# Kernel optimization log

Measured on AMD Instinct MI355X. Metric: run time of the kernel, lower is better.

The kernel has to match this reference:

```python
import jax, jax.numpy as jnp
import numpy as np

B, T, U = 4, 256, 64
D_ENC = D_PRED = 512
JOINT = 1024
VOCAB = 1024


def setup_inputs() -> dict:
    key = jax.random.key(0)
    ks = jax.random.split(key, 8)
    s = lambda d: 1.0 / np.sqrt(d)
    return {
        "enc": jax.random.normal(ks[0], (B, T, D_ENC), jnp.float32),
        "pred": jax.random.normal(ks[1], (B, U, D_PRED), jnp.float32),
        "W_enc": jax.random.normal(ks[2], (D_ENC, JOINT), jnp.float32) * s(D_ENC),
        "b_enc": jnp.zeros((JOINT,), jnp.float32),
        "W_pred": jax.random.normal(ks[3], (D_PRED, JOINT), jnp.float32) * s(D_PRED),
        "b_pred": jnp.zeros((JOINT,), jnp.float32),
        "W_out": jax.random.normal(ks[4], (JOINT, VOCAB), jnp.float32) * s(JOINT),
        "b_out": jnp.zeros((VOCAB,), jnp.float32),
    }


def reference(enc, pred, W_enc, b_enc, W_pred, b_pred, W_out, b_out):
    # Dense projections to joint_dim
    enc_out = jnp.einsum("btd,dj->btj", enc, W_enc) + b_enc      # [B,T,J]
    pred_out = jnp.einsum("bud,dj->buj", pred, W_pred) + b_pred  # [B,U,J]
    # Broadcast add over (T,U), tanh, then vocab projection
    joint = jnp.tanh(enc_out[:, :, None, :] + pred_out[:, None, :, :])  # [B,T,U,J]
    logits = jnp.einsum("btuj,jv->btuv", joint, W_out) + b_out           # [B,T,U,V]
    return logits
```

## Files before the change

kernel.cpp:

```cpp
#include <hip/hip_runtime.h>
#include <hip/hip_bf16.h>


typedef __bf16 bf16x8 __attribute__((ext_vector_type(8)));
typedef float f32x4 __attribute__((ext_vector_type(4)));
typedef unsigned int u32x4 __attribute__((ext_vector_type(4)));
using bf16_t = __hip_bfloat16;

#define B_ 4
#define T_ 256
#define U_ 64
#define DE 512
#define JD 1024
#define VV 1024

__device__ __forceinline__ void gl2lds16(const void* g, void* l) {
  __builtin_amdgcn_global_load_lds(
      (__attribute__((address_space(1))) void*)(g),
      (__attribute__((address_space(3))) void*)(l), 16, 0, 0);
}

__device__ __forceinline__ float fast_tanh(float x) {
  float xx = fminf(fmaxf(x, -30.f), 30.f);
  float e = __expf(2.f * xx);
  return 1.f - 2.f * __builtin_amdgcn_rcpf(e + 1.f);
}

__global__ void cvt_bf16_k(const float* __restrict__ src, bf16_t* __restrict__ dst, int n) {
  int i = (blockIdx.x * blockDim.x + threadIdx.x) * 4;
  if (i >= n) return;
  f32x4 v = *(const f32x4*)(src + i);
  bf16_t o[4];
#pragma unroll
  for (int z = 0; z < 4; ++z) o[z] = __float2bfloat16(v[z]);
  *(unsigned long long*)(dst + i) = *(unsigned long long*)o;
}

__global__ void transpose_cvt_k(const float* __restrict__ src, bf16_t* __restrict__ dst,
                                int K, int N) {
  __shared__ float tile[32][33];
  int nt = blockIdx.x * 32, kt = blockIdx.y * 32;
  int tx = threadIdx.x, ty = threadIdx.y;
#pragma unroll
  for (int i = 0; i < 4; ++i)
    tile[ty + i * 8][tx] = src[(size_t)(kt + ty + i * 8) * N + nt + tx];
  __syncthreads();
#pragma unroll
  for (int i = 0; i < 4; ++i)
    dst[(size_t)(nt + ty + i * 8) * K + kt + tx] = __float2bfloat16(tile[tx][ty + i * 8]);
}

__global__ __launch_bounds__(256) void tanh_mat_k(
    const float* __restrict__ enc_o,
    const float* __restrict__ pred_o,
    bf16_t* __restrict__ joint) {
  size_t i = ((size_t)blockIdx.x * 256 + threadIdx.x) * 8;
  const int m = (int)(i >> 10);
  const int j = (int)(i & 1023);
  const int enc_row  = m >> 6;
  const int pred_row = ((m >> 14) << 6) | (m & 63);
  const f32x4* pe = (const f32x4*)(enc_o  + (size_t)enc_row  * JD + j);
  const f32x4* pp = (const f32x4*)(pred_o + (size_t)pred_row * JD + j);
  bf16_t vals[8];
#pragma unroll
  for (int q = 0; q < 2; ++q) {
    f32x4 e = pe[q], p = pp[q];
#pragma unroll
    for (int z = 0; z < 4; ++z)
      vals[q * 4 + z] = __float2bfloat16(fast_tanh(e[z] + p[z]));
  }
  *(u32x4*)(void*)(joint + i) = *(const u32x4*)(const void*)vals;
}

__global__ __launch_bounds__(256) void proj_gemm_k(
    const bf16_t* __restrict__ A, const bf16_t* __restrict__ Bt,
    const float* __restrict__ bias, float* __restrict__ C, int M, int N, int K) {
  __shared__ bf16_t sA[128 * 32];
  __shared__ bf16_t sB[128 * 32];
  const int tid = threadIdx.x;
  const int wave = tid >> 6, lane = tid & 63;
  const int wm = wave >> 1, wn = wave & 1;
  const int m0 = blockIdx.y * 128, n0 = blockIdx.x * 128;

  f32x4 acc[4][4] = {};

  for (int k0 = 0; k0 < K; k0 += 32) {
    __syncthreads();
#pragma unroll
    for (int r = 0; r < 2; ++r) {
      const int base = (wave + 4 * r) * 1024;
      const int row  = (base >> 6) + (lane >> 2);
      const int kel  = (lane & 3) * 8;
      gl2lds16(A  + (size_t)(m0 + row) * K + k0 + kel, (char*)sA + base);
      gl2lds16(Bt + (size_t)(n0 + row) * K + k0 + kel, (char*)sB + base);
    }
    __syncthreads();
    bf16x8 af[4], bfr[4];
    const int kq = (lane >> 4) * 8;
#pragma unroll
    for (int i = 0; i < 4; ++i) {
      af[i]  = *(const bf16x8*)(const void*)(sA + (wm * 64 + i * 16 + (lane & 15)) * 32 + kq);
      bfr[i] = *(const bf16x8*)(const void*)(sB + (wn * 64 + i * 16 + (lane & 15)) * 32 + kq);
    }
#pragma unroll
    for (int i = 0; i < 4; ++i)
#pragma unroll
      for (int j = 0; j < 4; ++j)
        acc[i][j] = __builtin_amdgcn_mfma_f32_16x16x32_bf16(af[i], bfr[j], acc[i][j], 0, 0, 0);
  }

  float bv[4];
#pragma unroll
  for (int j = 0; j < 4; ++j) bv[j] = bias[n0 + wn * 64 + j * 16 + (lane & 15)];
#pragma unroll
  for (int i = 0; i < 4; ++i) {
    const int row = m0 + wm * 64 + i * 16 + ((lane >> 4) << 2);
#pragma unroll
    for (int j = 0; j < 4; ++j) {
      const int col = n0 + wn * 64 + j * 16 + (lane & 15);
#pragma unroll
      for (int rr = 0; rr < 4; ++rr)
        C[(size_t)(row + rr) * N + col] = acc[i][j][rr] + bv[j];
    }
  }
}


__device__ __forceinline__ void stage_vtile(const bf16_t* __restrict__ A,
                                            const bf16_t* __restrict__ Bt,
                                            int m0, int n0, int k0,
                                            char* buf, int wave, int lane) {
  char* ab = buf;
  char* bb = buf + 16384;
  const int rw = lane >> 2;
  const int cl = lane & 3;
#pragma unroll
  for (int g = 0; g < 2; ++g) {
    const int r  = g * 128 + wave * 16 + rw;
    const int cg = cl ^ ((r >> 1) & 3);
    gl2lds16(A  + (size_t)(m0 + r) * JD + k0 + cg * 8, ab + (g * 128 + wave * 16) * 64);
    gl2lds16(Bt + (size_t)(n0 + r) * JD + k0 + cg * 8, bb + (g * 128 + wave * 16) * 64);
  }
}

__global__ __launch_bounds__(512, 2) void vocab_gemm8_k(
    const bf16_t* __restrict__ A,
    const bf16_t* __restrict__ Bt,
    const float* __restrict__ bias,
    float* __restrict__ C) {
  __shared__ char smem[65536];
  const int tid  = threadIdx.x;
  const int wave = tid >> 6, lane = tid & 63;
  const int wm = wave >> 2, wn = wave & 3;

  const int nwg = gridDim.x;
  const int cpx = nwg >> 3;
  const int b   = blockIdx.x;
  const int lb  = (b & 7) * cpx + (b >> 3);
  const int n0  = (lb & 3) * 256;
  const int m0  = (lb >> 2) * 256;

  f32x4 acc[8][4] = {};

  const int NT = JD / 32;
  stage_vtile(A, Bt, m0, n0, 0,  smem,         wave, lane);
  stage_vtile(A, Bt, m0, n0, 32, smem + 32768, wave, lane);
  asm volatile("s_waitcnt vmcnt(4)" ::: "memory");
  __builtin_amdgcn_s_barrier();
  __builtin_amdgcn_sched_barrier(0);

  for (int t = 0; t < NT; ++t) {
    const char* ab = smem + (t & 1) * 32768;
    const char* bb = ab + 16384;
    const int kq = lane >> 4;

    bf16x8 bfr[4];
#pragma unroll
    for (int j = 0; j < 4; ++j) {
      const int rb = wn * 64 + j * 16 + (lane & 15);
      const int cb = kq ^ ((rb >> 1) & 3);
      bfr[j] = *(const bf16x8*)(const void*)(bb + rb * 64 + cb * 16);
    }
#pragma unroll
    for (int mh = 0; mh < 2; ++mh) {
      bf16x8 af[4];
#pragma unroll
      for (int i = 0; i < 4; ++i) {
        const int ra = wm * 128 + mh * 64 + i * 16 + (lane & 15);
        const int ca = kq ^ ((ra >> 1) & 3);
        af[i] = *(const bf16x8*)(const void*)(ab + ra * 64 + ca * 16);
      }
      __builtin_amdgcn_s_setprio(1);
#pragma unroll
      for (int i = 0; i < 4; ++i)
#pragma unroll
        for (int j = 0; j < 4; ++j)
          acc[mh * 4 + i][j] =
              __builtin_amdgcn_mfma_f32_16x16x32_bf16(af[i], bfr[j], acc[mh * 4 + i][j], 0, 0, 0);
      __builtin_amdgcn_s_setprio(0);
    }

    if (t + 1 < NT) {
      __builtin_amdgcn_sched_barrier(0);
      __builtin_amdgcn_s_barrier();
      if (t + 2 < NT) {
        stage_vtile(A, Bt, m0, n0, (t + 2) * 32, smem + (t & 1) * 32768, wave, lane);
        asm volatile("s_waitcnt vmcnt(4)" ::: "memory");
      } else {
        asm volatile("s_waitcnt vmcnt(0)" ::: "memory");
      }
      __builtin_amdgcn_s_barrier();
      __builtin_amdgcn_sched_barrier(0);
    }
  }

  float bv[4];
#pragma unroll
  for (int j = 0; j < 4; ++j) bv[j] = bias[n0 + wn * 64 + j * 16 + (lane & 15)];
#pragma unroll
  for (int i = 0; i < 8; ++i) {
    const int row = m0 + wm * 128 + i * 16 + ((lane >> 4) << 2);
#pragma unroll
    for (int j = 0; j < 4; ++j) {
      const int col = n0 + wn * 64 + j * 16 + (lane & 15);
#pragma unroll
      for (int rr = 0; rr < 4; ++rr)
        C[(size_t)(row + rr) * VV + col] = acc[i][j][rr] + bv[j];
    }
  }
}

__global__ __launch_bounds__(256) void joint_gemm_k(
    const float* __restrict__ enc_out,
    const float* __restrict__ pred_out,
    const bf16_t* __restrict__ Wt,
    const float* __restrict__ b_out,
    float* __restrict__ out) {
  __shared__ bf16_t sA[128 * 32];
  __shared__ bf16_t sB[128 * 32];
  const int tid = threadIdx.x;
  const int wave = tid >> 6, lane = tid & 63;
  const int wm = wave >> 1, wn = wave & 1;
  const int m0 = blockIdx.y * 128, n0 = blockIdx.x * 128;

  const int ar  = tid >> 1;
  const int ac0 = (tid & 1) * 16;
  const int m = m0 + ar;
  const int enc_row  = m >> 6;
  const int pred_row = ((m >> 14) << 6) | (m & 63);
  const float* pe_base = enc_out  + (size_t)enc_row  * JD + ac0;
  const float* pp_base = pred_out + (size_t)pred_row * JD + ac0;

  f32x4 acc[4][4] = {};

  for (int k0 = 0; k0 < JD; k0 += 32) {
    __syncthreads();
#pragma unroll
    for (int r = 0; r < 2; ++r) {
      const int base = (wave + 4 * r) * 1024;
      const int row  = (base >> 6) + (lane >> 2);
      const int kel  = (lane & 3) * 8;
      gl2lds16(Wt + (size_t)(n0 + row) * JD + k0 + kel, (char*)sB + base);
    }
    bf16_t vals[16];
    const f32x4* pe = (const f32x4*)(pe_base + k0);
    const f32x4* pp = (const f32x4*)(pp_base + k0);
#pragma unroll
    for (int q = 0; q < 4; ++q) {
      f32x4 e = pe[q], p = pp[q];
#pragma unroll
      for (int z = 0; z < 4; ++z)
        vals[q * 4 + z] = __float2bfloat16(fast_tanh(e[z] + p[z]));
    }
    u32x4* dstp = (u32x4*)(void*)((char*)sA + ar * 64 + ac0 * 2);
    dstp[0] = ((const u32x4*)(const void*)vals)[0];
    dstp[1] = ((const u32x4*)(const void*)vals)[1];
    __syncthreads();

    bf16x8 af[4], bfr[4];
    const int kq = (lane >> 4) * 8;
#pragma unroll
    for (int i = 0; i < 4; ++i) {
      af[i]  = *(const bf16x8*)(const void*)(sA + (wm * 64 + i * 16 + (lane & 15)) * 32 + kq);
      bfr[i] = *(const bf16x8*)(const void*)(sB + (wn * 64 + i * 16 + (lane & 15)) * 32 + kq);
    }
#pragma unroll
    for (int i = 0; i < 4; ++i)
#pragma unroll
      for (int j = 0; j < 4; ++j)
        acc[i][j] = __builtin_amdgcn_mfma_f32_16x16x32_bf16(af[i], bfr[j], acc[i][j], 0, 0, 0);
  }

  float bv[4];
#pragma unroll
  for (int j = 0; j < 4; ++j) bv[j] = b_out[n0 + wn * 64 + j * 16 + (lane & 15)];
#pragma unroll
  for (int i = 0; i < 4; ++i) {
    const int row = m0 + wm * 64 + i * 16 + ((lane >> 4) << 2);
#pragma unroll
    for (int j = 0; j < 4; ++j) {
      const int col = n0 + wn * 64 + j * 16 + (lane & 15);
#pragma unroll
      for (int rr = 0; rr < 4; ++rr)
        out[(size_t)(row + rr) * VV + col] = acc[i][j][rr] + bv[j];
    }
  }
}

extern "C" void kernel_launch(void* const* d_in, const int* in_sizes, int n_in,
                              void* d_out, int out_size, void* d_ws, size_t ws_size,
                              hipStream_t stream) {
  const float* enc    = (const float*)d_in[0];
  const float* pred   = (const float*)d_in[1];
  const float* W_enc  = (const float*)d_in[2];
  const float* b_enc  = (const float*)d_in[3];
  const float* W_pred = (const float*)d_in[4];
  const float* b_pred = (const float*)d_in[5];
  const float* W_out  = (const float*)d_in[6];
  const float* b_out  = (const float*)d_in[7];
  float* out = (float*)d_out;

  char* ws = (char*)d_ws;
  bf16_t* encb   = (bf16_t*)(ws + 0x000000);
  bf16_t* predb  = (bf16_t*)(ws + 0x100000);
  bf16_t* WtE    = (bf16_t*)(ws + 0x140000);
  bf16_t* WtP    = (bf16_t*)(ws + 0x240000);
  bf16_t* WtO    = (bf16_t*)(ws + 0x340000);
  float*  enc_o  = (float*) (ws + 0x540000);
  float*  pred_o = (float*) (ws + 0x940000);
  bf16_t* joint  = (bf16_t*)(ws + 0xA40000);
  const size_t WS_NEEDED = 0xA40000 + (size_t)(B_*T_*U_) * JD * sizeof(bf16_t);

  cvt_bf16_k<<<(B_*T_*DE) / 1024, 256, 0, stream>>>(enc, encb, B_*T_*DE);
  cvt_bf16_k<<<(B_*U_*DE) / 1024, 256, 0, stream>>>(pred, predb, B_*U_*DE);
  transpose_cvt_k<<<dim3(JD/32, DE/32), dim3(32, 8), 0, stream>>>(W_enc, WtE, DE, JD);
  transpose_cvt_k<<<dim3(JD/32, DE/32), dim3(32, 8), 0, stream>>>(W_pred, WtP, DE, JD);
  transpose_cvt_k<<<dim3(VV/32, JD/32), dim3(32, 8), 0, stream>>>(W_out, WtO, JD, VV);

  proj_gemm_k<<<dim3(JD/128, (B_*T_)/128), 256, 0, stream>>>(encb, WtE, b_enc, enc_o, B_*T_, JD, DE);
  proj_gemm_k<<<dim3(JD/128, (B_*U_)/128), 256, 0, stream>>>(predb, WtP, b_pred, pred_o, B_*U_, JD, DE);

  if (ws_size >= WS_NEEDED) {
    tanh_mat_k<<<(B_*T_*U_) * JD / (8 * 256), 256, 0, stream>>>(enc_o, pred_o, joint);
    vocab_gemm8_k<<<dim3(((B_*T_*U_) / 256) * (VV / 256)), 512, 0, stream>>>(
        joint, WtO, b_out, out);
  } else {
    joint_gemm_k<<<dim3(VV/128, (B_*T_*U_)/128), 256, 0, stream>>>(enc_o, pred_o, WtO, b_out, out);
  }
}
```

Baseline: 473.9 us.

## Fuse tanh joint into vocab GEMM and merge prep/projection launches

```diff
diff --git a/kernel.cpp b/kernel.cpp
--- a/kernel.cpp
+++ b/kernel.cpp
@@ -26,21 +26,12 @@
   return 1.f - 2.f * __builtin_amdgcn_rcpf(e + 1.f);
 }
 
-__global__ void cvt_bf16_k(const float* __restrict__ src, bf16_t* __restrict__ dst, int n) {
-  int i = (blockIdx.x * blockDim.x + threadIdx.x) * 4;
-  if (i >= n) return;
-  f32x4 v = *(const f32x4*)(src + i);
-  bf16_t o[4];
-#pragma unroll
-  for (int z = 0; z < 4; ++z) o[z] = __float2bfloat16(v[z]);
-  *(unsigned long long*)(dst + i) = *(unsigned long long*)o;
-}
-
-__global__ void transpose_cvt_k(const float* __restrict__ src, bf16_t* __restrict__ dst,
-                                int K, int N) {
-  __shared__ float tile[32][33];
-  int nt = blockIdx.x * 32, kt = blockIdx.y * 32;
-  int tx = threadIdx.x, ty = threadIdx.y;
+__device__ __forceinline__ void transpose_body(const float* __restrict__ src,
+                                               bf16_t* __restrict__ dst,
+                                               int K, int N, int bx, int by, int tid,
+                                               float (*tile)[33]) {
+  const int nt = bx * 32, kt = by * 32;
+  const int tx = tid & 31, ty = tid >> 5;
 #pragma unroll
   for (int i = 0; i < 4; ++i)
     tile[ty + i * 8][tx] = src[(size_t)(kt + ty + i * 8) * N + nt + tx];
@@ -50,37 +41,47 @@
     dst[(size_t)(nt + ty + i * 8) * K + kt + tx] = __float2bfloat16(tile[tx][ty + i * 8]);
 }
 
-__global__ __launch_bounds__(256) void tanh_mat_k(
-    const float* __restrict__ enc_o,
-    const float* __restrict__ pred_o,
-    bf16_t* __restrict__ joint) {
-  size_t i = ((size_t)blockIdx.x * 256 + threadIdx.x) * 8;
-  const int m = (int)(i >> 10);
-  const int j = (int)(i & 1023);
-  const int enc_row  = m >> 6;
-  const int pred_row = ((m >> 14) << 6) | (m & 63);
-  const f32x4* pe = (const f32x4*)(enc_o  + (size_t)enc_row  * JD + j);
-  const f32x4* pp = (const f32x4*)(pred_o + (size_t)pred_row * JD + j);
-  bf16_t vals[8];
-#pragma unroll
-  for (int q = 0; q < 2; ++q) {
-    f32x4 e = pe[q], p = pp[q];
-#pragma unroll
-    for (int z = 0; z < 4; ++z)
-      vals[q * 4 + z] = __float2bfloat16(fast_tanh(e[z] + p[z]));
-  }
-  *(u32x4*)(void*)(joint + i) = *(const u32x4*)(const void*)vals;
-}
-
-__global__ __launch_bounds__(256) void proj_gemm_k(
-    const bf16_t* __restrict__ A, const bf16_t* __restrict__ Bt,
-    const float* __restrict__ bias, float* __restrict__ C, int M, int N, int K) {
+__global__ __launch_bounds__(256) void prep_k(
+    const float* __restrict__ enc, const float* __restrict__ pred,
+    bf16_t* __restrict__ encb, bf16_t* __restrict__ predb,
+    const float* __restrict__ W_enc, bf16_t* __restrict__ WtE,
+    const float* __restrict__ W_pred, bf16_t* __restrict__ WtP,
+    const float* __restrict__ W_out, bf16_t* __restrict__ WtO) {
+  __shared__ float tile[32][33];
+  const int bid = blockIdx.x, tid = threadIdx.x;
+  if (bid < 640) {
+    size_t i = ((size_t)bid * 256 + tid) * 4;
+    const float* src;
+    bf16_t* dst;
+    if (i < (size_t)B_ * T_ * DE) { src = enc; dst = encb; }
+    else { i -= (size_t)B_ * T_ * DE; src = pred; dst = predb; }
+    f32x4 v = *(const f32x4*)(src + i);
+    bf16_t o[4];
+#pragma unroll
+    for (int z = 0; z < 4; ++z) o[z] = __float2bfloat16(v[z]);
+    *(unsigned long long*)(dst + i) = *(unsigned long long*)o;
+  } else if (bid < 1152) {
+    const int lb = bid - 640;
+    transpose_body(W_enc, WtE, DE, JD, lb & 31, lb >> 5, tid, tile);
+  } else if (bid < 1664) {
+    const int lb = bid - 1152;
+    transpose_body(W_pred, WtP, DE, JD, lb & 31, lb >> 5, tid, tile);
+  } else {
+    const int lb = bid - 1664;
+    transpose_body(W_out, WtO, JD, VV, lb & 31, lb >> 5, tid, tile);
+  }
+}
+
+__device__ __forceinline__ void proj_body(const bf16_t* __restrict__ A,
+                                          const bf16_t* __restrict__ Bt,
+                                          const float* __restrict__ bias,
+                                          float* __restrict__ C,
+                                          int m0, int n0, int N, int K) {
   __shared__ bf16_t sA[128 * 32];
   __shared__ bf16_t sB[128 * 32];
   const int tid = threadIdx.x;
   const int wave = tid >> 6, lane = tid & 63;
   const int wm = wave >> 1, wn = wave & 1;
-  const int m0 = blockIdx.y * 128, n0 = blockIdx.x * 128;
 
   f32x4 acc[4][4] = {};
 
@@ -125,26 +126,65 @@
   }
 }
 
-
-__device__ __forceinline__ void stage_vtile(const bf16_t* __restrict__ A,
-                                            const bf16_t* __restrict__ Bt,
-                                            int m0, int n0, int k0,
-                                            char* buf, int wave, int lane) {
-  char* ab = buf;
-  char* bb = buf + 16384;
+__global__ __launch_bounds__(256) void proj2_k(
+    const bf16_t* __restrict__ encb, const bf16_t* __restrict__ predb,
+    const bf16_t* __restrict__ WtE, const bf16_t* __restrict__ WtP,
+    const float* __restrict__ b_enc, const float* __restrict__ b_pred,
+    float* __restrict__ enc_o, float* __restrict__ pred_o) {
+  int bid = blockIdx.x;
+  if (bid < 64) {
+    proj_body(encb, WtE, b_enc, enc_o, (bid >> 3) * 128, (bid & 7) * 128, JD, DE);
+  } else {
+    bid -= 64;
+    proj_body(predb, WtP, b_pred, pred_o, (bid >> 3) * 128, (bid & 7) * 128, JD, DE);
+  }
+}
+
+
+__device__ __forceinline__ void stage_btile(const bf16_t* __restrict__ Bt,
+                                            int n0, int k0, char* bb, int wave, int lane) {
   const int rw = lane >> 2;
   const int cl = lane & 3;
 #pragma unroll
   for (int g = 0; g < 2; ++g) {
     const int r  = g * 128 + wave * 16 + rw;
     const int cg = cl ^ ((r >> 1) & 3);
-    gl2lds16(A  + (size_t)(m0 + r) * JD + k0 + cg * 8, ab + (g * 128 + wave * 16) * 64);
     gl2lds16(Bt + (size_t)(n0 + r) * JD + k0 + cg * 8, bb + (g * 128 + wave * 16) * 64);
   }
 }
 
-__global__ __launch_bounds__(512, 2) void vocab_gemm8_k(
-    const bf16_t* __restrict__ A,
+__device__ __forceinline__ void load_ep(const float* __restrict__ enc_o,
+                                        const float* __restrict__ pred_o,
+                                        int m0, int r, int h, int k0,
+                                        f32x4 e[4], f32x4 p[4]) {
+  const int m = m0 + r;
+  const int enc_row  = m >> 6;
+  const int pred_row = ((m >> 14) << 6) | (m & 63);
+  const float* pe = enc_o  + (size_t)enc_row  * JD + k0 + h * 16;
+  const float* pp = pred_o + (size_t)pred_row * JD + k0 + h * 16;
+#pragma unroll
+  for (int q = 0; q < 4; ++q) {
+    e[q] = *(const f32x4*)(pe + q * 4);
+    p[q] = *(const f32x4*)(pp + q * 4);
+  }
+}
+
+__device__ __forceinline__ void tanh_write_A(const f32x4 e[4], const f32x4 p[4],
+                                             char* ab, int r, int h) {
+  bf16_t vals[16];
+#pragma unroll
+  for (int q = 0; q < 4; ++q)
+#pragma unroll
+    for (int z = 0; z < 4; ++z)
+      vals[q * 4 + z] = __float2bfloat16(fast_tanh(e[q][z] + p[q][z]));
+  const int key = (r >> 1) & 3;
+  *(u32x4*)(void*)(ab + r * 64 + ((2 * h)     ^ key) * 16) = ((const u32x4*)(const void*)vals)[0];
+  *(u32x4*)(void*)(ab + r * 64 + ((2 * h + 1) ^ key) * 16) = ((const u32x4*)(const void*)vals)[1];
+}
+
+__global__ __launch_bounds__(512, 2) void vocab_fused_k(
+    const float* __restrict__ enc_o,
+    const float* __restrict__ pred_o,
     const bf16_t* __restrict__ Bt,
     const float* __restrict__ bias,
     float* __restrict__ C) {
@@ -153,25 +193,38 @@
   const int wave = tid >> 6, lane = tid & 63;
   const int wm = wave >> 2, wn = wave & 3;
 
-  const int nwg = gridDim.x;
-  const int cpx = nwg >> 3;
+  const int cpx = gridDim.x >> 3;
   const int b   = blockIdx.x;
   const int lb  = (b & 7) * cpx + (b >> 3);
   const int n0  = (lb & 3) * 256;
   const int m0  = (lb >> 2) * 256;
 
+  const int ar = tid >> 1;
+  const int ah = tid & 1;
+
   f32x4 acc[8][4] = {};
-
   const int NT = JD / 32;
-  stage_vtile(A, Bt, m0, n0, 0,  smem,         wave, lane);
-  stage_vtile(A, Bt, m0, n0, 32, smem + 32768, wave, lane);
-  asm volatile("s_waitcnt vmcnt(4)" ::: "memory");
+
+  {
+    f32x4 e[4], p[4];
+    load_ep(enc_o, pred_o, m0, ar, ah, 0, e, p);
+    tanh_write_A(e, p, smem, ar, ah);
+    load_ep(enc_o, pred_o, m0, ar, ah, 32, e, p);
+    tanh_write_A(e, p, smem + 16384, ar, ah);
+  }
+  stage_btile(Bt, n0, 0,  smem + 32768, wave, lane);
+  stage_btile(Bt, n0, 32, smem + 49152, wave, lane);
+  asm volatile("s_waitcnt vmcnt(2) lgkmcnt(0)" ::: "memory");
   __builtin_amdgcn_s_barrier();
   __builtin_amdgcn_sched_barrier(0);
 
+  f32x4 e2[4], p2[4];
+  load_ep(enc_o, pred_o, m0, ar, ah, 2 * 32, e2, p2);
+  __builtin_amdgcn_sched_barrier(0);
+
   for (int t = 0; t < NT; ++t) {
-    const char* ab = smem + (t & 1) * 32768;
-    const char* bb = ab + 16384;
+    const char* ab = smem + (t & 1) * 16384;
+    const char* bb = smem + 32768 + (t & 1) * 16384;
     const int kq = lane >> 4;
 
     bf16x8 bfr[4];
@@ -204,13 +257,18 @@
       __builtin_amdgcn_sched_barrier(0);
       __builtin_amdgcn_s_barrier();
       if (t + 2 < NT) {
-        stage_vtile(A, Bt, m0, n0, (t + 2) * 32, smem + (t & 1) * 32768, wave, lane);
-        asm volatile("s_waitcnt vmcnt(4)" ::: "memory");
+        stage_btile(Bt, n0, (t + 2) * 32, (char*)smem + 32768 + (t & 1) * 16384, wave, lane);
+        tanh_write_A(e2, p2, (char*)smem + (t & 1) * 16384, ar, ah);
+        asm volatile("s_waitcnt vmcnt(2) lgkmcnt(0)" ::: "memory");
       } else {
-        asm volatile("s_waitcnt vmcnt(0)" ::: "memory");
+        asm volatile("s_waitcnt vmcnt(0) lgkmcnt(0)" ::: "memory");
       }
       __builtin_amdgcn_s_barrier();
       __builtin_amdgcn_sched_barrier(0);
+      if (t + 3 < NT) {
+        load_ep(enc_o, pred_o, m0, ar, ah, (t + 3) * 32, e2, p2);
+        __builtin_amdgcn_sched_barrier(0);
+      }
     }
   }
 
@@ -226,83 +284,6 @@
 #pragma unroll
       for (int rr = 0; rr < 4; ++rr)
         C[(size_t)(row + rr) * VV + col] = acc[i][j][rr] + bv[j];
-    }
-  }
-}
-
-__global__ __launch_bounds__(256) void joint_gemm_k(
-    const float* __restrict__ enc_out,
-    const float* __restrict__ pred_out,
-    const bf16_t* __restrict__ Wt,
-    const float* __restrict__ b_out,
-    float* __restrict__ out) {
-  __shared__ bf16_t sA[128 * 32];
-  __shared__ bf16_t sB[128 * 32];
-  const int tid = threadIdx.x;
-  const int wave = tid >> 6, lane = tid & 63;
-  const int wm = wave >> 1, wn = wave & 1;
-  const int m0 = blockIdx.y * 128, n0 = blockIdx.x * 128;
-
-  const int ar  = tid >> 1;
-  const int ac0 = (tid & 1) * 16;
-  const int m = m0 + ar;
-  const int enc_row  = m >> 6;
-  const int pred_row = ((m >> 14) << 6) | (m & 63);
-  const float* pe_base = enc_out  + (size_t)enc_row  * JD + ac0;
-  const float* pp_base = pred_out + (size_t)pred_row * JD + ac0;
-
-  f32x4 acc[4][4] = {};
-
-  for (int k0 = 0; k0 < JD; k0 += 32) {
-    __syncthreads();
-#pragma unroll
-    for (int r = 0; r < 2; ++r) {
-      const int base = (wave + 4 * r) * 1024;
-      const int row  = (base >> 6) + (lane >> 2);
-      const int kel  = (lane & 3) * 8;
-      gl2lds16(Wt + (size_t)(n0 + row) * JD + k0 + kel, (char*)sB + base);
-    }
-    bf16_t vals[16];
-    const f32x4* pe = (const f32x4*)(pe_base + k0);
-    const f32x4* pp = (const f32x4*)(pp_base + k0);
-#pragma unroll
-    for (int q = 0; q < 4; ++q) {
-      f32x4 e = pe[q], p = pp[q];
-#pragma unroll
-      for (int z = 0; z < 4; ++z)
-        vals[q * 4 + z] = __float2bfloat16(fast_tanh(e[z] + p[z]));
-    }
-    u32x4* dstp = (u32x4*)(void*)((char*)sA + ar * 64 + ac0 * 2);
-    dstp[0] = ((const u32x4*)(const void*)vals)[0];
-    dstp[1] = ((const u32x4*)(const void*)vals)[1];
-    __syncthreads();
-
-    bf16x8 af[4], bfr[4];
-    const int kq = (lane >> 4) * 8;
-#pragma unroll
-    for (int i = 0; i < 4; ++i) {
-      af[i]  = *(const bf16x8*)(const void*)(sA + (wm * 64 + i * 16 + (lane & 15)) * 32 + kq);
-      bfr[i] = *(const bf16x8*)(const void*)(sB + (wn * 64 + i * 16 + (lane & 15)) * 32 + kq);
-    }
-#pragma unroll
-    for (int i = 0; i < 4; ++i)
-#pragma unroll
-      for (int j = 0; j < 4; ++j)
-        acc[i][j] = __builtin_amdgcn_mfma_f32_16x16x32_bf16(af[i], bfr[j], acc[i][j], 0, 0, 0);
-  }
-
-  float bv[4];
-#pragma unroll
-  for (int j = 0; j < 4; ++j) bv[j] = b_out[n0 + wn * 64 + j * 16 + (lane & 15)];
-#pragma unroll
-  for (int i = 0; i < 4; ++i) {
-    const int row = m0 + wm * 64 + i * 16 + ((lane >> 4) << 2);
-#pragma unroll
-    for (int j = 0; j < 4; ++j) {
-      const int col = n0 + wn * 64 + j * 16 + (lane & 15);
-#pragma unroll
-      for (int rr = 0; rr < 4; ++rr)
-        out[(size_t)(row + rr) * VV + col] = acc[i][j][rr] + bv[j];
     }
   }
 }
@@ -328,23 +309,11 @@
   bf16_t* WtO    = (bf16_t*)(ws + 0x340000);
   float*  enc_o  = (float*) (ws + 0x540000);
   float*  pred_o = (float*) (ws + 0x940000);
-  bf16_t* joint  = (bf16_t*)(ws + 0xA40000);
-  const size_t WS_NEEDED = 0xA40000 + (size_t)(B_*T_*U_) * JD * sizeof(bf16_t);
-
-  cvt_bf16_k<<<(B_*T_*DE) / 1024, 256, 0, stream>>>(enc, encb, B_*T_*DE);
-  cvt_bf16_k<<<(B_*U_*DE) / 1024, 256, 0, stream>>>(pred, predb, B_*U_*DE);
-  transpose_cvt_k<<<dim3(JD/32, DE/32), dim3(32, 8), 0, stream>>>(W_enc, WtE, DE, JD);
-  transpose_cvt_k<<<dim3(JD/32, DE/32), dim3(32, 8), 0, stream>>>(W_pred, WtP, DE, JD);
-  transpose_cvt_k<<<dim3(VV/32, JD/32), dim3(32, 8), 0, stream>>>(W_out, WtO, JD, VV);
-
-  proj_gemm_k<<<dim3(JD/128, (B_*T_)/128), 256, 0, stream>>>(encb, WtE, b_enc, enc_o, B_*T_, JD, DE);
-  proj_gemm_k<<<dim3(JD/128, (B_*U_)/128), 256, 0, stream>>>(predb, WtP, b_pred, pred_o, B_*U_, JD, DE);
-
-  if (ws_size >= WS_NEEDED) {
-    tanh_mat_k<<<(B_*T_*U_) * JD / (8 * 256), 256, 0, stream>>>(enc_o, pred_o, joint);
-    vocab_gemm8_k<<<dim3(((B_*T_*U_) / 256) * (VV / 256)), 512, 0, stream>>>(
-        joint, WtO, b_out, out);
-  } else {
-    joint_gemm_k<<<dim3(VV/128, (B_*T_*U_)/128), 256, 0, stream>>>(enc_o, pred_o, WtO, b_out, out);
-  }
-}
+
+  prep_k<<<2688, 256, 0, stream>>>(enc, pred, encb, predb, W_enc, WtE, W_pred, WtP, W_out, WtO);
+
+  proj2_k<<<80, 256, 0, stream>>>(encb, predb, WtE, WtP, b_enc, b_pred, enc_o, pred_o);
+
+  vocab_fused_k<<<dim3(((B_*T_*U_) / 256) * (VV / 256)), 512, 0, stream>>>(
+      enc_o, pred_o, WtO, b_out, out);
+}
```

Measured after the change: 496.7 us. 4.8% more time.
